# Kernel tuning notes

Hardware: AMD Instinct MI355X
Metric: run time of the kernel (lower is better)

## Reference

```python
import jax, jax.numpy as jnp
import numpy as np

N = 200_000      # nodes
E = 6_400_000    # edges (avg degree 32)
F = 128          # num_node_features
H = 96           # hidden_channels
G = 2_048        # number of graphs in batch


def setup_inputs() -> dict:
    key = jax.random.key(0)
    ks = jax.random.split(key, 12)
    def lin(k, fi, fo):
        kw, kb = jax.random.split(k)
        s = 1.0 / np.sqrt(fi)
        return (jax.random.uniform(kw, (fi, fo), jnp.float32, -s, s),
                jax.random.uniform(kb, (fo,), jnp.float32, -s, s))
    W1, b1 = lin(ks[0], F, H)
    W2, b2 = lin(ks[1], H, H)
    W3, b3 = lin(ks[2], H, H)
    Wl1, bl1 = lin(ks[3], H, H)
    Wl2, bl2 = lin(ks[4], H, 1)
    x = jax.random.normal(ks[5], (N, F), jnp.float32)
    edge_index = jax.random.randint(ks[6], (2, E), 0, N, jnp.int64)
    batch = jnp.sort(jax.random.randint(ks[7], (N,), 0, G, jnp.int64))
    return {"x": x, "W1": W1, "b1": b1, "W2": W2, "b2": b2, "W3": W3, "b3": b3,
            "Wl1": Wl1, "bl1": bl1, "Wl2": Wl2, "bl2": bl2,
            "edge_index": edge_index, "batch": batch}


def _gcn_layer(x, W, b, src, dst, norm):
    # transform then gather-scale-scatter (PyG GCNConv: bias added after aggregation)
    h = x @ W                                     # [N, out]
    msg = h[src] * norm[:, None]                  # [E+N, out]
    out = jax.ops.segment_sum(msg, dst, num_segments=N)
    return out + b


def reference(x, W1, b1, W2, b2, W3, b3, Wl1, bl1, Wl2, bl2, edge_index, batch):
    loops = jnp.arange(N, dtype=edge_index.dtype)
    src = jnp.concatenate([edge_index[0], loops])  # add self loops
    dst = jnp.concatenate([edge_index[1], loops])
    deg = jax.ops.segment_sum(jnp.ones_like(dst, dtype=x.dtype), dst, num_segments=N)
    dinv = jnp.where(deg > 0, deg ** -0.5, 0.0)
    norm = dinv[src] * dinv[dst]                   # symmetric D^-1/2 A D^-1/2

    h = jax.nn.relu(_gcn_layer(x, W1, b1, src, dst, norm))
    h = jax.nn.relu(_gcn_layer(h, W2, b2, src, dst, norm))
    h = _gcn_layer(h, W3, b3, src, dst, norm)
    # dropout(p=0.5) is identity in eval mode

    sums = jax.ops.segment_sum(h, batch, num_segments=G)        # [G, H]
    cnt = jax.ops.segment_sum(jnp.ones((N,), h.dtype), batch, num_segments=G)
    pooled = sums / jnp.maximum(cnt, 1.0)[:, None]              # global_mean_pool

    out = jax.nn.relu(pooled @ Wl1 + bl1)
    out = out @ Wl2 + bl2                                       # [G, 1]
    return out
```

## Files before the change

### kernel.cpp

```cpp
#include <hip/hip_runtime.h>
#include <hip/hip_bf16.h>
#include <hip/hip_fp16.h>
#include <cstdint>
#include <cstddef>


#define H96 96

static constexpr int NB_SHIFT = 8;
static constexpr int DPB = 1 << NB_SHIFT;
static constexpr int NBMAX = 800;
static constexpr int EPB = 8192;


__global__ __launch_bounds__(256, 4) void k_binscatter(
    const int* __restrict__ src, const int* __restrict__ dst, int E, int nb,
    int cap, int* __restrict__ gfill, unsigned* __restrict__ pairs) {
    __shared__ int cnt[NBMAX];
    const int tid = threadIdx.x;
    for (int b = tid; b < nb; b += 256) cnt[b] = 0;
    __syncthreads();

    const int base = blockIdx.x * EPB;
    int s[32], d[32];
#pragma unroll
    for (int q = 0; q < 32; ++q) {
        const int idx = base + q * 256 + tid;
        if (idx < E) {
            s[q] = src[idx];
            d[q] = dst[idx];
            atomicAdd(&cnt[d[q] >> NB_SHIFT], 1);
        } else {
            d[q] = -1;
        }
    }
    __syncthreads();
    for (int b = tid; b < nb; b += 256) {
        const int c = cnt[b];
        cnt[b] = (c > 0) ? atomicAdd(&gfill[b], c) : 0;
    }
    __syncthreads();
#pragma unroll
    for (int q = 0; q < 32; ++q) {
        if (d[q] >= 0) {
            const int b = d[q] >> NB_SHIFT;
            const int p = atomicAdd(&cnt[b], 1);
            if (p < cap)
                pairs[(size_t)b * cap + p] =
                    (unsigned)(s[q] & 0xFFFFFF) | ((unsigned)(d[q] & (DPB - 1)) << 24);
        }
    }
}

__global__ void k_bstart(const int* __restrict__ gfill, int* __restrict__ bstart, int nb) {
    __shared__ int sm[1024];
    const int tid = threadIdx.x;
    const int v = (tid < nb) ? gfill[tid] : 0;
    sm[tid] = v;
    __syncthreads();
    for (int o = 1; o < 1024; o <<= 1) {
        const int t = (tid >= o) ? sm[tid - o] : 0;
        __syncthreads();
        sm[tid] += t;
        __syncthreads();
    }
    if (tid < nb) bstart[tid] = sm[tid] - v;
    if (tid == 0) bstart[nb] = sm[1023];
}

__global__ __launch_bounds__(256) void k_build2(
    const unsigned* __restrict__ pairs, const int* __restrict__ gfill,
    const int* __restrict__ bstart, int cap, int* __restrict__ rowptr,
    float* __restrict__ dinv, int* __restrict__ csr, int N, int E) {
    __shared__ int cnt2[DPB];
    __shared__ int off2[DPB];
    const int b = blockIdx.x, tid = threadIdx.x;
    const int m = min(gfill[b], cap);
    const unsigned* pb = pairs + (size_t)b * cap;

    cnt2[tid] = 0;
    __syncthreads();
    for (int i = tid; i < m; i += 256) atomicAdd(&cnt2[pb[i] >> 24], 1);
    __syncthreads();

    const int v = cnt2[tid];
    off2[tid] = v;
    __syncthreads();
    for (int o = 1; o < 256; o <<= 1) {
        const int t = (tid >= o) ? off2[tid - o] : 0;
        __syncthreads();
        off2[tid] += t;
        __syncthreads();
    }
    const int excl = off2[tid] - v;
    const int base = bstart[b];
    const int dg = (b << NB_SHIFT) + tid;
    if (dg < N) {
        rowptr[dg] = base + excl;
        dinv[dg] = 1.0f / sqrtf((float)(v + 1));
    }
    if (b == 0 && tid == 0) rowptr[N] = E;
    __syncthreads();
    cnt2[tid] = excl;
    __syncthreads();
    for (int i = tid; i < m; i += 256) {
        const unsigned pk = pb[i];
        const int pos = base + atomicAdd(&cnt2[pk >> 24], 1);
        csr[pos] = (int)(pk & 0xFFFFFF);
    }
}


template <int K, int KC>
__global__ __launch_bounds__(384, 2) void k_gemm(const float* __restrict__ X,
                                                 const float* __restrict__ W,
                                                 const float* __restrict__ dinv,
                                                 __half* __restrict__ Out) {
    __shared__ float xs[64][KC + 4];
    __shared__ float ws[KC][H96];
    const int tid = threadIdx.x;
    const int nb = blockIdx.x * 64;
    const int tc = tid % 24;
    const int tn = tid / 24;

    float acc[4][4];
#pragma unroll
    for (int i = 0; i < 4; ++i)
#pragma unroll
        for (int c = 0; c < 4; ++c) acc[i][c] = 0.0f;

#pragma unroll 1
    for (int kc = 0; kc < K / KC; ++kc) {
#pragma unroll 1
        for (int idx = tid; idx < 64 * (KC / 4); idx += 384) {
            int row = idx / (KC / 4), kq = idx % (KC / 4);
            const float4 v = *(const float4*)&X[(size_t)(nb + row) * K + kc * KC + kq * 4];
            *(float4*)&xs[row][kq * 4] = v;
        }
#pragma unroll 1
        for (int idx = tid; idx < KC * 24; idx += 384) {
            int k = idx / 24, jq = idx % 24;
            const float4 v = *(const float4*)&W[(size_t)(kc * KC + k) * H96 + jq * 4];
            *(float4*)&ws[k][jq * 4] = v;
        }
        __syncthreads();

#pragma unroll 2
        for (int k = 0; k < KC; k += 4) {
            float4 wv[4];
#pragma unroll
            for (int kk = 0; kk < 4; ++kk) wv[kk] = *(float4*)&ws[k + kk][tc * 4];
#pragma unroll
            for (int i = 0; i < 4; ++i) {
                const float4 xq = *(float4*)&xs[tn * 4 + i][k];
                acc[i][0] = fmaf(xq.x, wv[0].x, acc[i][0]);
                acc[i][1] = fmaf(xq.x, wv[0].y, acc[i][1]);
                acc[i][2] = fmaf(xq.x, wv[0].z, acc[i][2]);
                acc[i][3] = fmaf(xq.x, wv[0].w, acc[i][3]);
                acc[i][0] = fmaf(xq.y, wv[1].x, acc[i][0]);
                acc[i][1] = fmaf(xq.y, wv[1].y, acc[i][1]);
                acc[i][2] = fmaf(xq.y, wv[1].z, acc[i][2]);
                acc[i][3] = fmaf(xq.y, wv[1].w, acc[i][3]);
                acc[i][0] = fmaf(xq.z, wv[2].x, acc[i][0]);
                acc[i][1] = fmaf(xq.z, wv[2].y, acc[i][1]);
                acc[i][2] = fmaf(xq.z, wv[2].z, acc[i][2]);
                acc[i][3] = fmaf(xq.z, wv[2].w, acc[i][3]);
                acc[i][0] = fmaf(xq.w, wv[3].x, acc[i][0]);
                acc[i][1] = fmaf(xq.w, wv[3].y, acc[i][1]);
                acc[i][2] = fmaf(xq.w, wv[3].z, acc[i][2]);
                acc[i][3] = fmaf(xq.w, wv[3].w, acc[i][3]);
            }
        }
        __syncthreads();
    }

    const int n0 = nb + tn * 4;
#pragma unroll
    for (int i = 0; i < 4; ++i) {
        const float sc = dinv[n0 + i];
        union { __half h[4]; uint2 u; } pk;
#pragma unroll
        for (int c = 0; c < 4; ++c) pk.h[c] = __float2half(acc[i][c] * sc);
        *(uint2*)&Out[(size_t)(n0 + i) * H96 + tc * 4] = pk.u;
    }
}


__global__ void k_agg(const __half* __restrict__ g, const int* __restrict__ rowptr,
                      const int* __restrict__ csr, const float* __restrict__ dinv,
                      const float* __restrict__ bias, float* __restrict__ hout,
                      int N, int RELU) {
    const int d = (blockIdx.x * blockDim.x + threadIdx.x) >> 6;
    if (d >= N) return;
    const int lane = threadIdx.x & 63;
    const int half = lane >> 5;
    const int l = lane & 31;

    float a0, a1, a2;
    if (half == 0) {
        const __half* gr = g + (size_t)d * H96;
        a0 = __half2float(gr[l]);
        a1 = __half2float(gr[l + 32]);
        a2 = __half2float(gr[l + 64]);
    } else {
        a0 = a1 = a2 = 0.0f;
    }
    float b0 = 0.f, b1 = 0.f, b2 = 0.f;
    float c0 = 0.f, c1 = 0.f, c2 = 0.f;
    float e0 = 0.f, e1 = 0.f, e2 = 0.f;

    const int r0 = rowptr[d], r1 = rowptr[d + 1];
    int e = r0 + half;
#pragma unroll 1
    for (; e + 6 < r1; e += 8) {
        const int s0 = csr[e];
        const int s1 = csr[e + 2];
        const int s2 = csr[e + 4];
        const int s3 = csr[e + 6];
        const __half* g0 = g + (size_t)s0 * H96;
        const __half* g1 = g + (size_t)s1 * H96;
        const __half* g2 = g + (size_t)s2 * H96;
        const __half* g3 = g + (size_t)s3 * H96;
        const float v00 = __half2float(g0[l]);
        const float v01 = __half2float(g0[l + 32]);
        const float v02 = __half2float(g0[l + 64]);
        const float v10 = __half2float(g1[l]);
        const float v11 = __half2float(g1[l + 32]);
        const float v12 = __half2float(g1[l + 64]);
        const float v20 = __half2float(g2[l]);
        const float v21 = __half2float(g2[l + 32]);
        const float v22 = __half2float(g2[l + 64]);
        const float v30 = __half2float(g3[l]);
        const float v31 = __half2float(g3[l + 32]);
        const float v32 = __half2float(g3[l + 64]);
        a0 += v00; a1 += v01; a2 += v02;
        b0 += v10; b1 += v11; b2 += v12;
        c0 += v20; c1 += v21; c2 += v22;
        e0 += v30; e1 += v31; e2 += v32;
    }
#pragma unroll 1
    for (; e < r1; e += 2) {
        const int s = csr[e];
        const __half* gs = g + (size_t)s * H96;
        a0 += __half2float(gs[l]);
        a1 += __half2float(gs[l + 32]);
        a2 += __half2float(gs[l + 64]);
    }
    a0 += (b0 + c0) + e0;
    a1 += (b1 + c1) + e1;
    a2 += (b2 + c2) + e2;

    a0 += __shfl_xor(a0, 32);
    a1 += __shfl_xor(a1, 32);
    a2 += __shfl_xor(a2, 32);

    if (half == 0) {
        const float sc = dinv[d];
        float v0 = sc * a0 + bias[l];
        float v1 = sc * a1 + bias[l + 32];
        float v2 = sc * a2 + bias[l + 64];
        if (RELU) { v0 = fmaxf(v0, 0.f); v1 = fmaxf(v1, 0.f); v2 = fmaxf(v2, 0.f); }
        float* ho = hout + (size_t)d * H96;
        ho[l] = v0; ho[l + 32] = v1; ho[l + 64] = v2;
    }
}


__global__ void k_pool_head(const float* __restrict__ h, const int* __restrict__ batch,
                            const float* __restrict__ Wl1, const float* __restrict__ bl1,
                            const float* __restrict__ Wl2, const float* __restrict__ bl2,
                            float* __restrict__ out, int N) {
    const int gph = blockIdx.x;
    const int tid = threadIdx.x;

    int lo = 0, hi = N;
    while (lo < hi) { int mid = (lo + hi) >> 1; if (batch[mid] < gph) lo = mid + 1; else hi = mid; }
    const int seg_lo = lo;
    lo = seg_lo; hi = N;
    while (lo < hi) { int mid = (lo + hi) >> 1; if (batch[mid] < gph + 1) lo = mid + 1; else hi = mid; }
    const int seg_hi = lo;

    __shared__ float pl[H96];
    __shared__ float prod[H96];
    const float inv_cnt = 1.0f / (float)max(seg_hi - seg_lo, 1);
    if (tid < H96) {
        float s = 0.0f;
        for (int n = seg_lo; n < seg_hi; ++n) s += h[(size_t)n * H96 + tid];
        pl[tid] = s * inv_cnt;
    }
    __syncthreads();
    if (tid < H96) {
        float hd = bl1[tid];
        for (int k = 0; k < H96; ++k) hd = fmaf(pl[k], Wl1[k * H96 + tid], hd);
        hd = fmaxf(hd, 0.0f);
        prod[tid] = hd * Wl2[tid];
    }
    __syncthreads();
    if (tid < 32) {
        float v = prod[tid] + prod[tid + 32] + prod[tid + 64];
        for (int o = 16; o; o >>= 1) v += __shfl_down(v, o);
        if (tid == 0) out[gph] = v + bl2[0];
    }
}


extern "C" void kernel_launch(void* const* d_in, const int* in_sizes, int n_in,
                              void* d_out, int out_size, void* d_ws, size_t ws_size,
                              hipStream_t stream) {
    const float* x   = (const float*)d_in[0];
    const float* W1  = (const float*)d_in[1];
    const float* b1  = (const float*)d_in[2];
    const float* W2  = (const float*)d_in[3];
    const float* b2  = (const float*)d_in[4];
    const float* W3  = (const float*)d_in[5];
    const float* b3  = (const float*)d_in[6];
    const float* Wl1 = (const float*)d_in[7];
    const float* bl1 = (const float*)d_in[8];
    const float* Wl2 = (const float*)d_in[9];
    const float* bl2 = (const float*)d_in[10];
    const int*   ei  = (const int*)d_in[11];
    const int*   bat = (const int*)d_in[12];

    const int N = in_sizes[0] / 128;
    const int E = in_sizes[11] / 2;
    const int G = out_size;
    const int* src = ei;
    const int* dst = ei + E;

    const int nb = (N + DPB - 1) >> NB_SHIFT;
    const int avg = E / nb;
    const int cap = (avg + (avg >> 3) + 1024 + 255) & ~255;

    char* wsb = (char*)d_ws;
    size_t off = 0;
    auto alloc = [&](size_t bytes) {
        void* p = wsb + off;
        off += (bytes + 255) & ~(size_t)255;
        return p;
    };
    __half*   g      = (__half*)alloc((size_t)N * H96 * 2);
    float*    h      = (float*)alloc((size_t)N * H96 * 4);
    int*      csr    = (int*)alloc((size_t)E * 4);
    int*      rowptr = (int*)alloc((size_t)(N + 1) * 4);
    float*    dinv   = (float*)alloc((size_t)N * 4);
    unsigned* pairs  = (unsigned*)alloc((size_t)nb * cap * 4);
    int*      gfill  = (int*)alloc((size_t)(nb + 1) * 4);
    int*      bstart = (int*)alloc((size_t)(nb + 1) * 4);

    hipMemsetAsync(gfill, 0, (size_t)nb * 4, stream);

    const int bs_blocks = (E + EPB - 1) / EPB;
    k_binscatter<<<bs_blocks, 256, 0, stream>>>(src, dst, E, nb, cap, gfill, pairs);
    k_bstart<<<1, 1024, 0, stream>>>(gfill, bstart, nb);
    k_build2<<<nb, 256, 0, stream>>>(pairs, gfill, bstart, cap, rowptr, dinv, csr, N, E);

    const int gemm_blocks = N / 64;
    const int agg_blocks = (N + 3) / 4;

    k_gemm<128, 64><<<gemm_blocks, 384, 0, stream>>>(x, W1, dinv, g);
    k_agg<<<agg_blocks, 256, 0, stream>>>(g, rowptr, csr, dinv, b1, h, N, 1);
    k_gemm<96, 48><<<gemm_blocks, 384, 0, stream>>>(h, W2, dinv, g);
    k_agg<<<agg_blocks, 256, 0, stream>>>(g, rowptr, csr, dinv, b2, h, N, 1);
    k_gemm<96, 48><<<gemm_blocks, 384, 0, stream>>>(h, W3, dinv, g);
    k_agg<<<agg_blocks, 256, 0, stream>>>(g, rowptr, csr, dinv, b3, h, N, 0);

    k_pool_head<<<G, 128, 0, stream>>>(h, bat, Wl1, bl1, Wl2, bl2, (float*)d_out, N);
}
```

Measured before the change: 1.075 ms.

## Split aggregation into three feature-slice passes with deeper gather unroll

The aggregation kernel now handles one 32-column slice of the 96-wide feature row per launch and is called three times per layer with different column offsets. Each pass has a smaller per-pass working set of the gathered half-precision table, which may raise cache hit rates for the random gathers, and the loop unroll grows to 8 outstanding edge loads. The cost is reading the CSR indices and rowptr three times and paying two extra launches per layer. Each gathered row segment is also only 64 bytes per slice, which is less efficient per memory transaction.

```diff
diff --git a/kernel.cpp b/kernel.cpp
--- a/kernel.cpp
+++ b/kernel.cpp
@@ -189,79 +189,51 @@
 __global__ void k_agg(const __half* __restrict__ g, const int* __restrict__ rowptr,
                       const int* __restrict__ csr, const float* __restrict__ dinv,
                       const float* __restrict__ bias, float* __restrict__ hout,
-                      int N, int RELU) {
+                      int N, int RELU, int fo) {
     const int d = (blockIdx.x * blockDim.x + threadIdx.x) >> 6;
     if (d >= N) return;
     const int lane = threadIdx.x & 63;
     const int half = lane >> 5;
-    const int l = lane & 31;
-
-    float a0, a1, a2;
-    if (half == 0) {
-        const __half* gr = g + (size_t)d * H96;
-        a0 = __half2float(gr[l]);
-        a1 = __half2float(gr[l + 32]);
-        a2 = __half2float(gr[l + 64]);
-    } else {
-        a0 = a1 = a2 = 0.0f;
-    }
-    float b0 = 0.f, b1 = 0.f, b2 = 0.f;
-    float c0 = 0.f, c1 = 0.f, c2 = 0.f;
-    float e0 = 0.f, e1 = 0.f, e2 = 0.f;
+    const int l = (lane & 31) + fo;
+
+    float a0 = (half == 0) ? __half2float(g[(size_t)d * H96 + l]) : 0.0f;
+    float a1 = 0.f, a2 = 0.f, a3 = 0.f;
+    float a4 = 0.f, a5 = 0.f, a6 = 0.f, a7 = 0.f;
 
     const int r0 = rowptr[d], r1 = rowptr[d + 1];
     int e = r0 + half;
 #pragma unroll 1
-    for (; e + 6 < r1; e += 8) {
+    for (; e + 14 < r1; e += 16) {
         const int s0 = csr[e];
         const int s1 = csr[e + 2];
         const int s2 = csr[e + 4];
         const int s3 = csr[e + 6];
-        const __half* g0 = g + (size_t)s0 * H96;
-        const __half* g1 = g + (size_t)s1 * H96;
-        const __half* g2 = g + (size_t)s2 * H96;
-        const __half* g3 = g + (size_t)s3 * H96;
-        const float v00 = __half2float(g0[l]);
-        const float v01 = __half2float(g0[l + 32]);
-        const float v02 = __half2float(g0[l + 64]);
-        const float v10 = __half2float(g1[l]);
-        const float v11 = __half2float(g1[l + 32]);
-        const float v12 = __half2float(g1[l + 64]);
-        const float v20 = __half2float(g2[l]);
-        const float v21 = __half2float(g2[l + 32]);
-        const float v22 = __half2float(g2[l + 64]);
-        const float v30 = __half2float(g3[l]);
-        const float v31 = __half2float(g3[l + 32]);
-        const float v32 = __half2float(g3[l + 64]);
-        a0 += v00; a1 += v01; a2 += v02;
-        b0 += v10; b1 += v11; b2 += v12;
-        c0 += v20; c1 += v21; c2 += v22;
-        e0 += v30; e1 += v31; e2 += v32;
+        const int s4 = csr[e + 8];
+        const int s5 = csr[e + 10];
+        const int s6 = csr[e + 12];
+        const int s7 = csr[e + 14];
+        const float v0 = __half2float(g[(size_t)s0 * H96 + l]);
+        const float v1 = __half2float(g[(size_t)s1 * H96 + l]);
+        const float v2 = __half2float(g[(size_t)s2 * H96 + l]);
+        const float v3 = __half2float(g[(size_t)s3 * H96 + l]);
+        const float v4 = __half2float(g[(size_t)s4 * H96 + l]);
+        const float v5 = __half2float(g[(size_t)s5 * H96 + l]);
+        const float v6 = __half2float(g[(size_t)s6 * H96 + l]);
+        const float v7 = __half2float(g[(size_t)s7 * H96 + l]);
+        a0 += v0; a1 += v1; a2 += v2; a3 += v3;
+        a4 += v4; a5 += v5; a6 += v6; a7 += v7;
     }
 #pragma unroll 1
     for (; e < r1; e += 2) {
-        const int s = csr[e];
-        const __half* gs = g + (size_t)s * H96;
-        a0 += __half2float(gs[l]);
-        a1 += __half2float(gs[l + 32]);
-        a2 += __half2float(gs[l + 64]);
-    }
-    a0 += (b0 + c0) + e0;
-    a1 += (b1 + c1) + e1;
-    a2 += (b2 + c2) + e2;
-
-    a0 += __shfl_xor(a0, 32);
-    a1 += __shfl_xor(a1, 32);
-    a2 += __shfl_xor(a2, 32);
+        a0 += __half2float(g[(size_t)csr[e] * H96 + l]);
+    }
+    float s = ((a0 + a1) + (a2 + a3)) + ((a4 + a5) + (a6 + a7));
+    s += __shfl_xor(s, 32);
 
     if (half == 0) {
-        const float sc = dinv[d];
-        float v0 = sc * a0 + bias[l];
-        float v1 = sc * a1 + bias[l + 32];
-        float v2 = sc * a2 + bias[l + 64];
-        if (RELU) { v0 = fmaxf(v0, 0.f); v1 = fmaxf(v1, 0.f); v2 = fmaxf(v2, 0.f); }
-        float* ho = hout + (size_t)d * H96;
-        ho[l] = v0; ho[l + 32] = v1; ho[l + 64] = v2;
+        float v = dinv[d] * s + bias[l];
+        if (RELU) v = fmaxf(v, 0.f);
+        hout[(size_t)d * H96 + l] = v;
     }
 }
 
@@ -358,11 +330,14 @@
     const int agg_blocks = (N + 3) / 4;
 
     k_gemm<128, 64><<<gemm_blocks, 384, 0, stream>>>(x, W1, dinv, g);
-    k_agg<<<agg_blocks, 256, 0, stream>>>(g, rowptr, csr, dinv, b1, h, N, 1);
+    for (int ph = 0; ph < 3; ++ph)
+        k_agg<<<agg_blocks, 256, 0, stream>>>(g, rowptr, csr, dinv, b1, h, N, 1, ph * 32);
     k_gemm<96, 48><<<gemm_blocks, 384, 0, stream>>>(h, W2, dinv, g);
-    k_agg<<<agg_blocks, 256, 0, stream>>>(g, rowptr, csr, dinv, b2, h, N, 1);
+    for (int ph = 0; ph < 3; ++ph)
+        k_agg<<<agg_blocks, 256, 0, stream>>>(g, rowptr, csr, dinv, b2, h, N, 1, ph * 32);
     k_gemm<96, 48><<<gemm_blocks, 384, 0, stream>>>(h, W3, dinv, g);
-    k_agg<<<agg_blocks, 256, 0, stream>>>(g, rowptr, csr, dinv, b3, h, N, 0);
+    for (int ph = 0; ph < 3; ++ph)
+        k_agg<<<agg_blocks, 256, 0, stream>>>(g, rowptr, csr, dinv, b3, h, N, 0, ph * 32);
 
     k_pool_head<<<G, 128, 0, stream>>>(h, bat, Wl1, bl1, Wl2, bl2, (float*)d_out, N);
 }
```

Result: slower. 1.771 ms (+64.7%).

## Use MFMA fp16 GEMM and store intermediate activations in half precision

Applied to the files above, without the earlier changes.

Replaces the FP32 scalar-FMA tiled GEMM with a kernel built on the 16x16x32 f16 MFMA instruction. The weights are transposed into fp16 shared memory, and each wave loads its A fragments straight from global memory. The aggregation output h is now stored as fp16 instead of fp32, which halves the write traffic in aggregation and the read traffic in the next GEMM and in pooling. The cost is lower precision in the weights, activations and hidden features. The output stores are also scattered per element as 2-byte writes.

```diff
diff --git a/kernel.cpp b/kernel.cpp
--- a/kernel.cpp
+++ b/kernel.cpp
@@ -3,9 +3,13 @@
 #include <hip/hip_fp16.h>
 #include <cstdint>
 #include <cstddef>
+#include <type_traits>
 
 
 #define H96 96
+
+typedef _Float16 f16x8 __attribute__((ext_vector_type(8)));
+typedef float f32x4 __attribute__((ext_vector_type(4)));
 
 static constexpr int NB_SHIFT = 8;
 static constexpr int DPB = 1 << NB_SHIFT;
@@ -111,84 +115,67 @@
 }
 
 
-template <int K, int KC>
-__global__ __launch_bounds__(384, 2) void k_gemm(const float* __restrict__ X,
-                                                 const float* __restrict__ W,
-                                                 const float* __restrict__ dinv,
-                                                 __half* __restrict__ Out) {
-    __shared__ float xs[64][KC + 4];
-    __shared__ float ws[KC][H96];
+template <int K, typename AT>
+__global__ __launch_bounds__(256) void k_gemm_mfma(const AT* __restrict__ X,
+                                                   const float* __restrict__ W,
+                                                   const float* __restrict__ dinv,
+                                                   __half* __restrict__ Out) {
+    __shared__ _Float16 wt[H96][K + 8];
     const int tid = threadIdx.x;
-    const int nb = blockIdx.x * 64;
-    const int tc = tid % 24;
-    const int tn = tid / 24;
-
-    float acc[4][4];
-#pragma unroll
-    for (int i = 0; i < 4; ++i)
-#pragma unroll
-        for (int c = 0; c < 4; ++c) acc[i][c] = 0.0f;
-
-#pragma unroll 1
-    for (int kc = 0; kc < K / KC; ++kc) {
-#pragma unroll 1
-        for (int idx = tid; idx < 64 * (KC / 4); idx += 384) {
-            int row = idx / (KC / 4), kq = idx % (KC / 4);
-            const float4 v = *(const float4*)&X[(size_t)(nb + row) * K + kc * KC + kq * 4];
-            *(float4*)&xs[row][kq * 4] = v;
+    const int l = tid & 63;
+    const int w = tid >> 6;
+
+    for (int idx = tid; idx < K * H96; idx += 256) {
+        const int k = idx / H96, j = idx % H96;
+        wt[j][k] = (_Float16)W[idx];
+    }
+    __syncthreads();
+
+    const int g16 = l >> 4;
+    const int rl = l & 15;
+    const size_t n0 = (size_t)blockIdx.x * 64 + w * 16;
+
+    f32x4 acc[6];
+#pragma unroll
+    for (int c = 0; c < 6; ++c) acc[c] = (f32x4){0.f, 0.f, 0.f, 0.f};
+
+#pragma unroll
+    for (int kk = 0; kk < K / 32; ++kk) {
+        const int k0 = kk * 32 + g16 * 8;
+        f16x8 a;
+        if constexpr (std::is_same<AT, float>::value) {
+            const float* xr = X + (n0 + rl) * K + k0;
+            const float4 lo = *(const float4*)xr;
+            const float4 hi = *(const float4*)(xr + 4);
+            a[0] = (_Float16)lo.x; a[1] = (_Float16)lo.y;
+            a[2] = (_Float16)lo.z; a[3] = (_Float16)lo.w;
+            a[4] = (_Float16)hi.x; a[5] = (_Float16)hi.y;
+            a[6] = (_Float16)hi.z; a[7] = (_Float16)hi.w;
+        } else {
+            a = *(const f16x8*)((const _Float16*)X + (n0 + rl) * K + k0);
         }
-#pragma unroll 1
-        for (int idx = tid; idx < KC * 24; idx += 384) {
-            int k = idx / 24, jq = idx % 24;
-            const float4 v = *(const float4*)&W[(size_t)(kc * KC + k) * H96 + jq * 4];
-            *(float4*)&ws[k][jq * 4] = v;
+#pragma unroll
+        for (int c = 0; c < 6; ++c) {
+            const f16x8 b = *(const f16x8*)&wt[c * 16 + rl][k0];
+            acc[c] = __builtin_amdgcn_mfma_f32_16x16x32_f16(a, b, acc[c], 0, 0, 0);
         }
-        __syncthreads();
-
-#pragma unroll 2
-        for (int k = 0; k < KC; k += 4) {
-            float4 wv[4];
-#pragma unroll
-            for (int kk = 0; kk < 4; ++kk) wv[kk] = *(float4*)&ws[k + kk][tc * 4];
-#pragma unroll
-            for (int i = 0; i < 4; ++i) {
-                const float4 xq = *(float4*)&xs[tn * 4 + i][k];
-                acc[i][0] = fmaf(xq.x, wv[0].x, acc[i][0]);
-                acc[i][1] = fmaf(xq.x, wv[0].y, acc[i][1]);
-                acc[i][2] = fmaf(xq.x, wv[0].z, acc[i][2]);
-                acc[i][3] = fmaf(xq.x, wv[0].w, acc[i][3]);
-                acc[i][0] = fmaf(xq.y, wv[1].x, acc[i][0]);
-                acc[i][1] = fmaf(xq.y, wv[1].y, acc[i][1]);
-                acc[i][2] = fmaf(xq.y, wv[1].z, acc[i][2]);
-                acc[i][3] = fmaf(xq.y, wv[1].w, acc[i][3]);
-                acc[i][0] = fmaf(xq.z, wv[2].x, acc[i][0]);
-                acc[i][1] = fmaf(xq.z, wv[2].y, acc[i][1]);
-                acc[i][2] = fmaf(xq.z, wv[2].z, acc[i][2]);
-                acc[i][3] = fmaf(xq.z, wv[2].w, acc[i][3]);
-                acc[i][0] = fmaf(xq.w, wv[3].x, acc[i][0]);
-                acc[i][1] = fmaf(xq.w, wv[3].y, acc[i][1]);
-                acc[i][2] = fmaf(xq.w, wv[3].z, acc[i][2]);
-                acc[i][3] = fmaf(xq.w, wv[3].w, acc[i][3]);
-            }
-        }
-        __syncthreads();
-    }
-
-    const int n0 = nb + tn * 4;
-#pragma unroll
-    for (int i = 0; i < 4; ++i) {
-        const float sc = dinv[n0 + i];
-        union { __half h[4]; uint2 u; } pk;
-#pragma unroll
-        for (int c = 0; c < 4; ++c) pk.h[c] = __float2half(acc[i][c] * sc);
-        *(uint2*)&Out[(size_t)(n0 + i) * H96 + tc * 4] = pk.u;
-    }
+    }
+
+    const int r0 = g16 * 4;
+    float dv[4];
+#pragma unroll
+    for (int r = 0; r < 4; ++r) dv[r] = dinv[n0 + r0 + r];
+#pragma unroll
+    for (int c = 0; c < 6; ++c)
+#pragma unroll
+        for (int r = 0; r < 4; ++r)
+            Out[(n0 + r0 + r) * H96 + c * 16 + rl] = __float2half(acc[c][r] * dv[r]);
 }
 
 
 __global__ void k_agg(const __half* __restrict__ g, const int* __restrict__ rowptr,
                       const int* __restrict__ csr, const float* __restrict__ dinv,
-                      const float* __restrict__ bias, float* __restrict__ hout,
+                      const float* __restrict__ bias, __half* __restrict__ hout,
                       int N, int RELU) {
     const int d = (blockIdx.x * blockDim.x + threadIdx.x) >> 6;
     if (d >= N) return;
@@ -260,13 +247,15 @@
         float v1 = sc * a1 + bias[l + 32];
         float v2 = sc * a2 + bias[l + 64];
         if (RELU) { v0 = fmaxf(v0, 0.f); v1 = fmaxf(v1, 0.f); v2 = fmaxf(v2, 0.f); }
-        float* ho = hout + (size_t)d * H96;
-        ho[l] = v0; ho[l + 32] = v1; ho[l + 64] = v2;
-    }
-}
-
-
-__global__ void k_pool_head(const float* __restrict__ h, const int* __restrict__ batch,
+        __half* ho = hout + (size_t)d * H96;
+        ho[l] = __float2half(v0);
+        ho[l + 32] = __float2half(v1);
+        ho[l + 64] = __float2half(v2);
+    }
+}
+
+
+__global__ void k_pool_head(const __half* __restrict__ h, const int* __restrict__ batch,
                             const float* __restrict__ Wl1, const float* __restrict__ bl1,
                             const float* __restrict__ Wl2, const float* __restrict__ bl2,
                             float* __restrict__ out, int N) {
@@ -285,7 +274,7 @@
     const float inv_cnt = 1.0f / (float)max(seg_hi - seg_lo, 1);
     if (tid < H96) {
         float s = 0.0f;
-        for (int n = seg_lo; n < seg_hi; ++n) s += h[(size_t)n * H96 + tid];
+        for (int n = seg_lo; n < seg_hi; ++n) s += __half2float(h[(size_t)n * H96 + tid]);
         pl[tid] = s * inv_cnt;
     }
     __syncthreads();
@@ -339,7 +328,7 @@
         return p;
     };
     __half*   g      = (__half*)alloc((size_t)N * H96 * 2);
-    float*    h      = (float*)alloc((size_t)N * H96 * 4);
+    __half*   h      = (__half*)alloc((size_t)N * H96 * 2);
     int*      csr    = (int*)alloc((size_t)E * 4);
     int*      rowptr = (int*)alloc((size_t)(N + 1) * 4);
     float*    dinv   = (float*)alloc((size_t)N * 4);
@@ -357,11 +346,11 @@
     const int gemm_blocks = N / 64;
     const int agg_blocks = (N + 3) / 4;
 
-    k_gemm<128, 64><<<gemm_blocks, 384, 0, stream>>>(x, W1, dinv, g);
+    k_gemm_mfma<128, float><<<gemm_blocks, 256, 0, stream>>>(x, W1, dinv, g);
     k_agg<<<agg_blocks, 256, 0, stream>>>(g, rowptr, csr, dinv, b1, h, N, 1);
-    k_gemm<96, 48><<<gemm_blocks, 384, 0, stream>>>(h, W2, dinv, g);
+    k_gemm_mfma<96, __half><<<gemm_blocks, 256, 0, stream>>>(h, W2, dinv, g);
     k_agg<<<agg_blocks, 256, 0, stream>>>(g, rowptr, csr, dinv, b2, h, N, 1);
-    k_gemm<96, 48><<<gemm_blocks, 384, 0, stream>>>(h, W3, dinv, g);
+    k_gemm_mfma<96, __half><<<gemm_blocks, 256, 0, stream>>>(h, W3, dinv, g);
     k_agg<<<agg_blocks, 256, 0, stream>>>(g, rowptr, csr, dinv, b3, h, N, 0);
 
     k_pool_head<<<G, 128, 0, stream>>>(h, bat, Wl1, bl1, Wl2, bl2, (float*)d_out, N);
```

After: 910.0 us (median of 3 runs). 15.4% less time.
